# Performance work log

Measured on AMD Instinct MI355X. Metric: run time of the kernel, lower is better.

The kernel has to match this reference:

```python
import jax, jax.numpy as jnp
import numpy as np

MEM_LEN = 1024
EPS = 1e-5


def _layer_norm(x, g, b):
    mu = jnp.mean(x, axis=-1, keepdims=True)
    var = jnp.mean((x - mu) ** 2, axis=-1, keepdims=True)
    return (x - mu) * jax.lax.rsqrt(var + EPS) * g + b


def _rel_shift(t):
    # t: [B, H, T, L] -> TXL pad->view->slice->view shift
    B, H, T, L = t.shape
    padded = jnp.concatenate([jnp.zeros((B, H, T, 1), t.dtype), t], axis=-1)
    padded = padded.reshape(B, H, L + 1, T)
    return padded[:, :, 1:, :].reshape(B, H, T, L)


def _pos_emb(length, d_model, dtype):
    inv_freq = 1.0 / (10000.0 ** (np.arange(0, d_model, 2, dtype=np.float32) / d_model))
    pos_seq = np.arange(length - 1, -1, -1, dtype=np.float32)
    sin_inp = np.outer(pos_seq, inv_freq)
    pe = np.concatenate([np.sin(sin_inp), np.cos(sin_inp)], axis=-1)
    return jnp.asarray(pe, dtype=dtype)


def setup_inputs() -> dict:
    key = jax.random.key(0)
    ks = jax.random.split(key, 12)
    B, T, M, D, H, Dff = 4, 1024, 1024, 1024, 16, 4096
    dh = D // H
    s = 1.0 / np.sqrt(D)
    return {
        "x": jax.random.normal(ks[0], (B, T, D), jnp.float32),
        "mem": jax.random.normal(ks[1], (B, M, D), jnp.float32),
        "Wq": jax.random.normal(ks[2], (D, D), jnp.float32) * s,
        "Wk": jax.random.normal(ks[3], (D, D), jnp.float32) * s,
        "Wv": jax.random.normal(ks[4], (D, D), jnp.float32) * s,
        "Wr": jax.random.normal(ks[5], (D, D), jnp.float32) * s,
        "Wo": jax.random.normal(ks[6], (D, D), jnp.float32) * s,
        "bias_u": jax.random.normal(ks[7], (H, dh), jnp.float32) * 0.02,
        "bias_v": jax.random.normal(ks[8], (H, dh), jnp.float32) * 0.02,
        "ln1_g": jnp.ones((D,), jnp.float32),
        "ln1_b": jnp.zeros((D,), jnp.float32),
        "ln2_g": jnp.ones((D,), jnp.float32),
        "ln2_b": jnp.zeros((D,), jnp.float32),
        "W1": jax.random.normal(ks[9], (D, Dff), jnp.float32) * s,
        "b1": jnp.zeros((Dff,), jnp.float32),
        "W2": jax.random.normal(ks[10], (Dff, D), jnp.float32) * (1.0 / np.sqrt(Dff)),
        "b2": jnp.zeros((D,), jnp.float32),
    }


def reference(x, mem, Wq, Wk, Wv, Wr, Wo, bias_u, bias_v,
              ln1_g, ln1_b, ln2_g, ln2_b, W1, b1, W2, b2):
    B, T, D = x.shape
    M = mem.shape[1]
    H, dh = bias_u.shape
    L = T + M
    scale = 1.0 / np.sqrt(dh)

    residual = x
    xn = _layer_norm(x, ln1_g, ln1_b)

    cat = jnp.concatenate([mem_n := mem, xn], axis=1) if False else jnp.concatenate([mem, xn], axis=1)
    # NOTE: torch concatenates raw memory states (not re-normalized) with norm_x.
    k = (cat @ Wk).reshape(B, L, H, dh).transpose(0, 2, 1, 3)      # [B,H,L,dh]
    v = (cat @ Wv).reshape(B, L, H, dh).transpose(0, 2, 1, 3)      # [B,H,L,dh]
    q = (xn @ Wq).reshape(B, T, H, dh).transpose(0, 2, 1, 3)       # [B,H,T,dh]

    pe = _pos_emb(L, D, x.dtype)                                   # [L,D]
    r = (pe @ Wr).reshape(L, H, dh).transpose(1, 0, 2)             # [H,L,dh]

    content = jnp.einsum("bhid,bhjd->bhij", q + bias_u[None, :, None, :], k)
    rel = jnp.einsum("bhid,hjd->bhij", q + bias_v[None, :, None, :], r)
    rel = _rel_shift(rel)

    attn = jax.nn.softmax((content + rel) * scale, axis=-1)        # [B,H,T,L]
    out = jnp.einsum("bhij,bhjd->bhid", attn, v)                   # [B,H,T,dh]
    out = out.transpose(0, 2, 1, 3).reshape(B, T, D) @ Wo

    x2 = residual + out
    xf = _layer_norm(x2, ln2_g, ln2_b)
    ff = jax.nn.gelu(xf @ W1 + b1, approximate=False) @ W2 + b2
    y = x2 + ff

    new_mem = jax.lax.stop_gradient(
        jnp.concatenate([mem, residual], axis=1)[:, -MEM_LEN:])
    return y, new_mem
```

## Files before the change

kernel.cpp:

```cpp
#include <hip/hip_runtime.h>
#include <hip/hip_bf16.h>

typedef short bf16x8 __attribute__((ext_vector_type(8)));
typedef float f32x4 __attribute__((ext_vector_type(4)));
typedef unsigned short u16;

__device__ __forceinline__ float bf2f(u16 u) {
    union { unsigned int i; float f; } x; x.i = ((unsigned int)u) << 16; return x.f;
}
__device__ __forceinline__ u16 f2bf(float f) {
    union { float f; unsigned int i; } x; x.f = f;
    unsigned int r = x.i + 0x7fff + ((x.i >> 16) & 1);
    return (u16)(r >> 16);
}
__device__ __forceinline__ f32x4 mfma16(bf16x8 a, bf16x8 b, f32x4 c) {
    return __builtin_amdgcn_mfma_f32_16x16x32_bf16(a, b, c, 0, 0, 0);
}
#define GLL16(lds_base, gsrc) \
    __builtin_amdgcn_global_load_lds((const __attribute__((address_space(1))) void*)(gsrc), \
                                     (__attribute__((address_space(3))) void*)(lds_base), 16, 0, 0)

__global__ __launch_bounds__(256)
void transpose_kernel(const float* __restrict__ in, u16* __restrict__ out, int R, int C) {
    __shared__ float t[32][33];
    const int c0 = blockIdx.x * 32, r0 = blockIdx.y * 32;
    const int tx = threadIdx.x & 31, ty = threadIdx.x >> 5;
#pragma unroll
    for (int i = 0; i < 32; i += 8) t[ty + i][tx] = in[(size_t)(r0 + ty + i) * C + c0 + tx];
    __syncthreads();
#pragma unroll
    for (int i = 0; i < 32; i += 8) out[(size_t)(c0 + ty + i) * R + r0 + tx] = f2bf(t[tx][ty + i]);
}

__global__ __launch_bounds__(256)
void convert_kernel(const float* __restrict__ in, u16* __restrict__ out) {
    const size_t i = ((size_t)blockIdx.x * 256 + threadIdx.x) * 8;
    const float4 a = *(const float4*)(in + i);
    const float4 b = *(const float4*)(in + i + 4);
    bf16x8 o;
    o[0] = (short)f2bf(a.x); o[1] = (short)f2bf(a.y);
    o[2] = (short)f2bf(a.z); o[3] = (short)f2bf(a.w);
    o[4] = (short)f2bf(b.x); o[5] = (short)f2bf(b.y);
    o[6] = (short)f2bf(b.z); o[7] = (short)f2bf(b.w);
    *(bf16x8*)(out + i) = o;
}

__global__ __launch_bounds__(256)
void pe_kernel(u16* __restrict__ pe) {
    const int idx = blockIdx.x * 256 + threadIdx.x;
    const int p = idx >> 10, d = idx & 1023;
    const float pos = (float)(2047 - p);
    const int k = d & 511;
    const float invf = powf(10000.f, ((float)(2 * k)) * (-1.f / 1024.f));
    const float a = pos * invf;
    pe[idx] = f2bf((d < 512) ? sinf(a) : cosf(a));
}

__global__ __launch_bounds__(256)
void ln_kernel(const float* __restrict__ inp, const float* __restrict__ gg,
               const float* __restrict__ bb, u16* __restrict__ outp) {
    const int row = blockIdx.x * 4 + (threadIdx.x >> 6);
    const int l = threadIdx.x & 63;
    const size_t base = (size_t)row * 1024 + l * 16;
    float v[16];
    const float4* p4 = (const float4*)(inp + base);
#pragma unroll
    for (int j = 0; j < 4; ++j) {
        float4 f = p4[j];
        v[j*4+0] = f.x; v[j*4+1] = f.y; v[j*4+2] = f.z; v[j*4+3] = f.w;
    }
    float s = 0.f, s2 = 0.f;
#pragma unroll
    for (int j = 0; j < 16; ++j) { s += v[j]; s2 += v[j] * v[j]; }
#pragma unroll
    for (int off = 1; off < 64; off <<= 1) {
        s += __shfl_xor(s, off, 64);
        s2 += __shfl_xor(s2, off, 64);
    }
    const float mu = s * 0.0009765625f;
    const float var = s2 * 0.0009765625f - mu * mu;
    const float rs = rsqrtf(var + 1e-5f);
#pragma unroll
    for (int j = 0; j < 16; ++j)
        outp[base + j] = f2bf((v[j] - mu) * rs * gg[l * 16 + j] + bb[l * 16 + j]);
}

template<int EPI, bool CATA>
__global__ __launch_bounds__(256)
void gemm_kernel(const u16* __restrict__ A, const u16* __restrict__ A2,
                 const u16* __restrict__ Wt, void* __restrict__ outp,
                 u16* __restrict__ out2, const float* __restrict__ cb1,
                 const float* __restrict__ cb2, const float* __restrict__ residp,
                 int Mdim, int Ndim, int Kdim) {
    __shared__ __attribute__((aligned(16))) u16 As[128 * 32];
    __shared__ __attribute__((aligned(16))) u16 Bs[128 * 32];
    const int tid = threadIdx.x;
    const int w = tid >> 6, l = tid & 63;
    const int wr = w >> 1, wc = w & 1;
    const int m0 = blockIdx.x * 128, n0 = blockIdx.y * 128;
    f32x4 acc[4][4] = {};

    for (int k0 = 0; k0 < Kdim; k0 += 32) {
        __syncthreads();
#pragma unroll
        for (int p = 0; p < 2; ++p) {
            const int ebase = (p * 4 + w) * 512;
            const int e = ebase + l * 8;
            const int row = e >> 5, colk = e & 31;
            const u16* srcA;
            if (CATA) {
                const int rr = m0 + row;
                const int bb_ = rr >> 11, pos = rr & 2047;
                srcA = (pos < 1024 ? A + ((size_t)(bb_ * 1024 + pos)) * 1024
                                   : A2 + ((size_t)(bb_ * 1024 + pos - 1024)) * 1024)
                       + (k0 + colk);
            } else {
                srcA = A + (size_t)(m0 + row) * Kdim + (k0 + colk);
            }
            const u16* srcB = Wt + (size_t)(n0 + row) * Kdim + (k0 + colk);
            GLL16(&As[ebase], srcA);
            GLL16(&Bs[ebase], srcB);
        }
        __syncthreads();
        bf16x8 af[4], bfr[4];
#pragma unroll
        for (int mi = 0; mi < 4; ++mi)
            af[mi] = *(const bf16x8*)&As[(wr * 64 + mi * 16 + (l & 15)) * 32 + (l >> 4) * 8];
#pragma unroll
        for (int ni = 0; ni < 4; ++ni)
            bfr[ni] = *(const bf16x8*)&Bs[(wc * 64 + ni * 16 + (l & 15)) * 32 + (l >> 4) * 8];
#pragma unroll
        for (int mi = 0; mi < 4; ++mi)
#pragma unroll
            for (int ni = 0; ni < 4; ++ni)
                acc[mi][ni] = mfma16(af[mi], bfr[ni], acc[mi][ni]);
    }

#pragma unroll
    for (int mi = 0; mi < 4; ++mi)
#pragma unroll
        for (int ni = 0; ni < 4; ++ni)
#pragma unroll
            for (int rg = 0; rg < 4; ++rg) {
                const int row = m0 + wr * 64 + mi * 16 + (l >> 4) * 4 + rg;
                const int col = n0 + wc * 64 + ni * 16 + (l & 15);
                const size_t idx = (size_t)row * Ndim + col;
                const float v = acc[mi][ni][rg];
                if (EPI == 0) {
                    ((u16*)outp)[idx] = f2bf(v);
                } else if (EPI == 1) {
                    ((u16*)outp)[idx] = f2bf(v + cb1[col]);
                    out2[idx] = f2bf(v + cb2[col]);
                } else if (EPI == 2) {
                    ((float*)outp)[idx] = v + residp[idx];
                } else if (EPI == 3) {
                    const float t = v + cb1[col];
                    ((u16*)outp)[idx] = f2bf(0.5f * t * (1.f + erff(t * 0.70710678118654752f)));
                } else {
                    ((float*)outp)[idx] = v + cb1[col] + residp[idx];
                }
            }
}

template<int EPI>
__global__ __launch_bounds__(256)
void gemm64_kernel(const u16* __restrict__ A, const u16* __restrict__ Wt,
                   void* __restrict__ outp, u16* __restrict__ out2,
                   const float* __restrict__ cb1, const float* __restrict__ cb2,
                   const float* __restrict__ residp,
                   int Mdim, int Ndim, int Kdim) {
    __shared__ __attribute__((aligned(16))) u16 As[64 * 32];
    __shared__ __attribute__((aligned(16))) u16 Bs[128 * 32];
    const int tid = threadIdx.x;
    const int w = tid >> 6, l = tid & 63;
    const int m0 = blockIdx.x * 64, n0 = blockIdx.y * 128;
    f32x4 acc[4][2] = {};

    for (int k0 = 0; k0 < Kdim; k0 += 32) {
        __syncthreads();
        {
            const int e = (w * 64 + l) * 8;
            const int row = e >> 5, colk = e & 31;
            GLL16(&As[w * 512], A + (size_t)(m0 + row) * Kdim + (k0 + colk));
        }
#pragma unroll
        for (int p = 0; p < 2; ++p) {
            const int ebase = (p * 4 + w) * 512;
            const int e = ebase + l * 8;
            const int row = e >> 5, colk = e & 31;
            GLL16(&Bs[ebase], Wt + (size_t)(n0 + row) * Kdim + (k0 + colk));
        }
        __syncthreads();
        bf16x8 af[4], bfr[2];
#pragma unroll
        for (int mi = 0; mi < 4; ++mi)
            af[mi] = *(const bf16x8*)&As[(mi * 16 + (l & 15)) * 32 + (l >> 4) * 8];
#pragma unroll
        for (int ni = 0; ni < 2; ++ni)
            bfr[ni] = *(const bf16x8*)&Bs[(w * 32 + ni * 16 + (l & 15)) * 32 + (l >> 4) * 8];
#pragma unroll
        for (int mi = 0; mi < 4; ++mi)
#pragma unroll
            for (int ni = 0; ni < 2; ++ni)
                acc[mi][ni] = mfma16(af[mi], bfr[ni], acc[mi][ni]);
    }

#pragma unroll
    for (int mi = 0; mi < 4; ++mi)
#pragma unroll
        for (int ni = 0; ni < 2; ++ni)
#pragma unroll
            for (int rg = 0; rg < 4; ++rg) {
                const int row = m0 + mi * 16 + (l >> 4) * 4 + rg;
                const int col = n0 + w * 32 + ni * 16 + (l & 15);
                const size_t idx = (size_t)row * Ndim + col;
                const float v = acc[mi][ni][rg];
                if (EPI == 0) {
                    ((u16*)outp)[idx] = f2bf(v);
                } else if (EPI == 1) {
                    ((u16*)outp)[idx] = f2bf(v + cb1[col]);
                    out2[idx] = f2bf(v + cb2[col]);
                } else if (EPI == 2) {
                    ((float*)outp)[idx] = v + residp[idx];
                } else {
                    ((float*)outp)[idx] = v + cb1[col] + residp[idx];
                }
            }
}

__global__ __launch_bounds__(256)
void gemm_kv_kernel(const u16* __restrict__ A, const u16* __restrict__ A2,
                    const u16* __restrict__ WtK, const u16* __restrict__ WtV,
                    u16* __restrict__ outK, u16* __restrict__ outV) {
    __shared__ __attribute__((aligned(16))) u16 As[128 * 32];
    __shared__ __attribute__((aligned(16))) u16 Bk[128 * 32];
    __shared__ __attribute__((aligned(16))) u16 Bv[128 * 32];
    const int tid = threadIdx.x;
    const int w = tid >> 6, l = tid & 63;
    const int wr = w >> 1, wc = w & 1;
    const int m0 = blockIdx.x * 128, n0 = blockIdx.y * 128;
    f32x4 acck[4][4] = {};
    f32x4 accv[4][4] = {};

    for (int k0 = 0; k0 < 1024; k0 += 32) {
        __syncthreads();
#pragma unroll
        for (int p = 0; p < 2; ++p) {
            const int ebase = (p * 4 + w) * 512;
            const int e = ebase + l * 8;
            const int row = e >> 5, colk = e & 31;
            const int rr = m0 + row;
            const int bb_ = rr >> 11, pos = rr & 2047;
            const u16* srcA = (pos < 1024 ? A + ((size_t)(bb_ * 1024 + pos)) * 1024
                                          : A2 + ((size_t)(bb_ * 1024 + pos - 1024)) * 1024)
                              + (k0 + colk);
            GLL16(&As[ebase], srcA);
            GLL16(&Bk[ebase], WtK + (size_t)(n0 + row) * 1024 + (k0 + colk));
            GLL16(&Bv[ebase], WtV + (size_t)(n0 + row) * 1024 + (k0 + colk));
        }
        __syncthreads();
        bf16x8 af[4], bkf[4], bvf[4];
#pragma unroll
        for (int mi = 0; mi < 4; ++mi)
            af[mi] = *(const bf16x8*)&As[(wr * 64 + mi * 16 + (l & 15)) * 32 + (l >> 4) * 8];
#pragma unroll
        for (int ni = 0; ni < 4; ++ni) {
            const int off = (wc * 64 + ni * 16 + (l & 15)) * 32 + (l >> 4) * 8;
            bkf[ni] = *(const bf16x8*)&Bk[off];
            bvf[ni] = *(const bf16x8*)&Bv[off];
        }
#pragma unroll
        for (int mi = 0; mi < 4; ++mi)
#pragma unroll
            for (int ni = 0; ni < 4; ++ni) {
                acck[mi][ni] = mfma16(af[mi], bkf[ni], acck[mi][ni]);
                accv[mi][ni] = mfma16(af[mi], bvf[ni], accv[mi][ni]);
            }
    }

#pragma unroll
    for (int mi = 0; mi < 4; ++mi)
#pragma unroll
        for (int ni = 0; ni < 4; ++ni)
#pragma unroll
            for (int rg = 0; rg < 4; ++rg) {
                const int row = m0 + wr * 64 + mi * 16 + (l >> 4) * 4 + rg;
                const int col = n0 + wc * 64 + ni * 16 + (l & 15);
                const size_t idx = (size_t)row * 1024 + col;
                outK[idx] = f2bf(acck[mi][ni][rg]);
                outV[idx] = f2bf(accv[mi][ni][rg]);
            }
}

__global__ __launch_bounds__(256, 2)
void attn_kernel(const u16* __restrict__ qu, const u16* __restrict__ qv,
                 const u16* __restrict__ kcat, const u16* __restrict__ vcat,
                 const u16* __restrict__ rbuf, u16* __restrict__ outp) {
    constexpr int T = 1024, L = 2048, MM = 1024;
    __shared__ __attribute__((aligned(16))) u16 KtL[64 * 64];
    __shared__ __attribute__((aligned(16))) u16 RmL[128 * 64];
    __shared__ __attribute__((aligned(16))) u16 RwL[128 * 64];
    __shared__ __attribute__((aligned(16))) u16 Vt[64][72];
    __shared__ __attribute__((aligned(16))) u16 Pl[4][16][72];
    const int bid = blockIdx.x;
    const int g = (bid & 7) + 8 * (bid >> 7);
    const int it = (bid >> 3) & 15;
    const int h = g & 15, b = g >> 4;
    const int i0 = it * 64;
    const int tid = threadIdx.x;
    const int w = tid >> 6, l = tid & 63;
    const int lg = l >> 4, ll = l & 15;
    const int iw0 = i0 + w * 16;
    const int l8 = l >> 3;
    const int ssrc = ((l & 7) * 8) ^ (l8 << 3);
    const int sA = (lg * 8) ^ ((ll & 7) << 3);
    const int sB = (lg * 8 + 32) ^ ((ll & 7) << 3);

    bf16x8 quf[2], qvf[2];
    const int qc = h * 64 + lg * 8;
    {
        const size_t qrow = (size_t)(b * T + iw0 + ll);
        quf[0] = *(const bf16x8*)&qu[qrow * 1024 + qc];
        quf[1] = *(const bf16x8*)&qu[qrow * 1024 + qc + 32];
        qvf[0] = *(const bf16x8*)&qv[qrow * 1024 + qc];
        qvf[1] = *(const bf16x8*)&qv[qrow * 1024 + qc + 32];
    }
    const int r2 = iw0 + ll + 1;
    const size_t qrow2 = (size_t)(b * T + (r2 < T ? r2 : T - 1));
    const u16* kb = kcat + (size_t)b * L * 1024 + h * 64;
    const u16* vb = vcat + (size_t)b * L * 1024 + h * 64;
    const u16* rb = rbuf + h * 64;

    f32x4 o_acc[4] = {};
    float m_run[4] = {-1e30f, -1e30f, -1e30f, -1e30f};
    float l_run[4] = {0.f, 0.f, 0.f, 0.f};
    const int vjq = tid & 15, vdg = tid >> 4;

    for (int jt = 0; jt < 32; ++jt) {
        const int j0 = jt * 64;
        const bool main_blk = (j0 <= MM + i0 + 63);
        const bool wrap_blk = (j0 + 63 >= MM + i0 + 2);
        __syncthreads();
#pragma unroll
        for (int p = 0; p < 2; ++p) {
            const int k8 = w * 2 + p;
            GLL16(&KtL[k8 * 512], kb + (size_t)(j0 + k8 * 8 + l8) * 1024 + ssrc);
        }
        if (main_blk) {
            const long bm = (long)j0 + T - i0 - 64;
#pragma unroll
            for (int p = 0; p < 4; ++p) {
                const int k8 = w * 4 + p;
                GLL16(&RmL[k8 * 512], rb + (long)(bm + k8 * 8 + l8) * 1024 + ssrc);
            }
        }
        if (wrap_blk) {
            const long bw_ = (long)j0 - MM - i0 - 65;
#pragma unroll
            for (int p = 0; p < 4; ++p) {
                const int k8 = w * 4 + p;
                GLL16(&RwL[k8 * 512], rb + (long)(bw_ + k8 * 8 + l8) * 1024 + ssrc);
            }
        }
        {
            const u16* srcv = vb + (size_t)(j0 + vjq * 4) * 1024 + vdg * 4;
            const ushort4 r0 = *(const ushort4*)(srcv);
            const ushort4 r1 = *(const ushort4*)(srcv + 1024);
            const ushort4 r2w = *(const ushort4*)(srcv + 2048);
            const ushort4 r3 = *(const ushort4*)(srcv + 3072);
            const ushort4 c0 = {r0.x, r1.x, r2w.x, r3.x};
            const ushort4 c1 = {r0.y, r1.y, r2w.y, r3.y};
            const ushort4 c2 = {r0.z, r1.z, r2w.z, r3.z};
            const ushort4 c3 = {r0.w, r1.w, r2w.w, r3.w};
            *(ushort4*)&Vt[vdg * 4 + 0][vjq * 4] = c0;
            *(ushort4*)&Vt[vdg * 4 + 1][vjq * 4] = c1;
            *(ushort4*)&Vt[vdg * 4 + 2][vjq * 4] = c2;
            *(ushort4*)&Vt[vdg * 4 + 3][vjq * 4] = c3;
        }
        __syncthreads();

        f32x4 sv[4];
        __builtin_amdgcn_s_setprio(1);
#pragma unroll
        for (int ns = 0; ns < 4; ++ns) {
            const int rowb = (ns * 16 + ll) * 64;
            f32x4 a = {0.f, 0.f, 0.f, 0.f};
            a = mfma16(quf[0], *(const bf16x8*)&KtL[rowb + sA], a);
            a = mfma16(quf[1], *(const bf16x8*)&KtL[rowb + sB], a);
            sv[ns] = a;
        }
        __builtin_amdgcn_s_setprio(0);

        if (j0 <= MM + iw0 + 15) {
            const int trb = 48 - 16 * w;
            f32x4 gb[5];
#pragma unroll
            for (int cs = 0; cs < 5; ++cs) {
                const int rowb = (trb + cs * 16 + ll) * 64;
                f32x4 a = {0.f, 0.f, 0.f, 0.f};
                a = mfma16(qvf[0], *(const bf16x8*)&RmL[rowb + sA], a);
                a = mfma16(qvf[1], *(const bf16x8*)&RmL[rowb + sB], a);
                gb[cs] = a;
            }
#pragma unroll
            for (int r = 0; r < 4; ++r) {
                const int i_loc = lg * 4 + r;
                const int srcl = (l & 48) | ((ll + 15 - i_loc) & 15);
                const float sh0 = __shfl(gb[0][r], srcl, 64);
                const float sh1 = __shfl(gb[1][r], srcl, 64);
                const float sh2 = __shfl(gb[2][r], srcl, 64);
                const float sh3 = __shfl(gb[3][r], srcl, 64);
                const float sh4 = __shfl(gb[4][r], srcl, 64);
                const bool hi = (ll > i_loc);
                const int thr = MM + iw0 + i_loc - j0;
                const float e0 = hi ? sh1 : sh0;
                const float e1 = hi ? sh2 : sh1;
                const float e2 = hi ? sh3 : sh2;
                const float e3 = hi ? sh4 : sh3;
                if (ll <= thr)      sv[0][r] += e0;
                if (16 + ll <= thr) sv[1][r] += e1;
                if (32 + ll <= thr) sv[2][r] += e2;
                if (48 + ll <= thr) sv[3][r] += e3;
            }
        }
        if (j0 + 63 >= MM + iw0 + 2) {
            const bf16x8 qv2f0 = *(const bf16x8*)&qv[qrow2 * 1024 + qc];
            const bf16x8 qv2f1 = *(const bf16x8*)&qv[qrow2 * 1024 + qc + 32];
            const int trb = 48 - 16 * w;
            f32x4 gb[5];
#pragma unroll
            for (int cs = 0; cs < 5; ++cs) {
                const int rowb = (trb + cs * 16 + ll) * 64;
                f32x4 a = {0.f, 0.f, 0.f, 0.f};
                a = mfma16(qv2f0, *(const bf16x8*)&RwL[rowb + sA], a);
                a = mfma16(qv2f1, *(const bf16x8*)&RwL[rowb + sB], a);
                gb[cs] = a;
            }
#pragma unroll
            for (int r = 0; r < 4; ++r) {
                const int i_loc = lg * 4 + r;
                const int srcl = (l & 48) | ((ll + 15 - i_loc) & 15);
                const float sh0 = __shfl(gb[0][r], srcl, 64);
                const float sh1 = __shfl(gb[1][r], srcl, 64);
                const float sh2 = __shfl(gb[2][r], srcl, 64);
                const float sh3 = __shfl(gb[3][r], srcl, 64);
                const float sh4 = __shfl(gb[4][r], srcl, 64);
                const bool hi = (ll > i_loc);
                const int thr2 = MM + iw0 + i_loc - j0 + 2;
                const float e0 = hi ? sh1 : sh0;
                const float e1 = hi ? sh2 : sh1;
                const float e2 = hi ? sh3 : sh2;
                const float e3 = hi ? sh4 : sh3;
                if (ll >= thr2)      sv[0][r] += e0;
                if (16 + ll >= thr2) sv[1][r] += e1;
                if (32 + ll >= thr2) sv[2][r] += e2;
                if (48 + ll >= thr2) sv[3][r] += e3;
            }
        }

#pragma unroll
        for (int r = 0; r < 4; ++r) {
            const int i_loc = lg * 4 + r;
            const float s0 = sv[0][r] * 0.125f, s1 = sv[1][r] * 0.125f;
            const float s2 = sv[2][r] * 0.125f, s3 = sv[3][r] * 0.125f;
            float pm = fmaxf(fmaxf(s0, s1), fmaxf(s2, s3));
            pm = fmaxf(pm, __shfl_xor(pm, 1, 64));
            pm = fmaxf(pm, __shfl_xor(pm, 2, 64));
            pm = fmaxf(pm, __shfl_xor(pm, 4, 64));
            pm = fmaxf(pm, __shfl_xor(pm, 8, 64));
            const float mnew = fmaxf(m_run[r], pm);
            const float alpha = __expf(m_run[r] - mnew);
            const float p0 = __expf(s0 - mnew), p1 = __expf(s1 - mnew);
            const float p2 = __expf(s2 - mnew), p3 = __expf(s3 - mnew);
            Pl[w][i_loc][0 * 16 + ll] = f2bf(p0);
            Pl[w][i_loc][1 * 16 + ll] = f2bf(p1);
            Pl[w][i_loc][2 * 16 + ll] = f2bf(p2);
            Pl[w][i_loc][3 * 16 + ll] = f2bf(p3);
            float ps = p0 + p1 + p2 + p3;
            ps += __shfl_xor(ps, 1, 64);
            ps += __shfl_xor(ps, 2, 64);
            ps += __shfl_xor(ps, 4, 64);
            ps += __shfl_xor(ps, 8, 64);
            l_run[r] = l_run[r] * alpha + ps;
            m_run[r] = mnew;
#pragma unroll
            for (int ns = 0; ns < 4; ++ns) o_acc[ns][r] *= alpha;
        }

        __builtin_amdgcn_s_setprio(1);
        const bf16x8 ap0 = *(const bf16x8*)&Pl[w][ll][lg * 8];
        const bf16x8 ap1 = *(const bf16x8*)&Pl[w][ll][32 + lg * 8];
#pragma unroll
        for (int ns = 0; ns < 4; ++ns) {
            const bf16x8 bv0 = *(const bf16x8*)&Vt[ns * 16 + ll][lg * 8];
            const bf16x8 bv1 = *(const bf16x8*)&Vt[ns * 16 + ll][32 + lg * 8];
            o_acc[ns] = mfma16(ap0, bv0, o_acc[ns]);
            o_acc[ns] = mfma16(ap1, bv1, o_acc[ns]);
        }
        __builtin_amdgcn_s_setprio(0);
    }

#pragma unroll
    for (int ns = 0; ns < 4; ++ns)
#pragma unroll
        for (int r = 0; r < 4; ++r) {
            const int row = iw0 + lg * 4 + r;
            outp[(size_t)(b * T + row) * 1024 + h * 64 + ns * 16 + ll] =
                f2bf(o_acc[ns][r] / l_run[r]);
        }
}

extern "C" void kernel_launch(void* const* d_in, const int* in_sizes, int n_in,
                              void* d_out, int out_size, void* d_ws, size_t ws_size,
                              hipStream_t stream) {
    const float* x    = (const float*)d_in[0];
    const float* mem  = (const float*)d_in[1];
    const float* Wq   = (const float*)d_in[2];
    const float* Wk   = (const float*)d_in[3];
    const float* Wv   = (const float*)d_in[4];
    const float* Wr   = (const float*)d_in[5];
    const float* Wo   = (const float*)d_in[6];
    const float* bu   = (const float*)d_in[7];
    const float* bv   = (const float*)d_in[8];
    const float* ln1g = (const float*)d_in[9];
    const float* ln1b = (const float*)d_in[10];
    const float* ln2g = (const float*)d_in[11];
    const float* ln2b = (const float*)d_in[12];
    const float* W1   = (const float*)d_in[13];
    const float* b1   = (const float*)d_in[14];
    const float* W2   = (const float*)d_in[15];
    const float* b2   = (const float*)d_in[16];

    float* y_out   = (float*)d_out;
    float* mem_out = (float*)d_out + 4194304;

    char* dob = (char*)d_out;
    u16* attno     = (u16*)(dob + 0);
    u16* pe        = (u16*)(dob + (size_t)8  * 1048576);
    u16* rbuf_base = (u16*)(dob + (size_t)12 * 1048576);
    u16* rbuf      = rbuf_base + 80 * 1024;
    char* dw = dob + (size_t)16 * 1048576 + 524288;
    u16* WqT = (u16*)(dw);
    u16* WkT = (u16*)(dw + (size_t)2 * 1048576);
    u16* WvT = (u16*)(dw + (size_t)4 * 1048576);
    u16* WrT = (u16*)(dw + (size_t)6 * 1048576);
    u16* WoT = (u16*)(dw + (size_t)8 * 1048576);

    char* ws = (char*)d_ws;
    const size_t MB = 1u << 20;
    u16*  xn    = (u16*)(ws + 0 * MB);
    u16*  x2n   = (u16*)(ws + 0 * MB);
    u16*  W2T   = (u16*)(ws + 0 * MB);
    u16*  qu    = (u16*)(ws + 8 * MB);
    float* x2f  = (float*)(ws + 8 * MB);
    u16*  qv    = (u16*)(ws + 16 * MB);
    u16*  kcat  = (u16*)(ws + 24 * MB);
    u16*  ffh   = (u16*)(ws + 24 * MB);
    u16*  vcat  = (u16*)(ws + 40 * MB);
    u16*  memb  = (u16*)(ws + 56 * MB);
    u16*  W1T   = (u16*)(ws + 56 * MB);

    transpose_kernel<<<dim3(32, 32), 256, 0, stream>>>(Wq, WqT, 1024, 1024);
    transpose_kernel<<<dim3(32, 32), 256, 0, stream>>>(Wk, WkT, 1024, 1024);
    transpose_kernel<<<dim3(32, 32), 256, 0, stream>>>(Wv, WvT, 1024, 1024);
    transpose_kernel<<<dim3(32, 32), 256, 0, stream>>>(Wr, WrT, 1024, 1024);
    transpose_kernel<<<dim3(32, 32), 256, 0, stream>>>(Wo, WoT, 1024, 1024);
    pe_kernel<<<8192, 256, 0, stream>>>(pe);
    convert_kernel<<<2048, 256, 0, stream>>>(mem, memb);
    ln_kernel<<<1024, 256, 0, stream>>>(x, ln1g, ln1b, xn);
    gemm64_kernel<0><<<dim3(32, 8), 256, 0, stream>>>(pe, WrT, rbuf, nullptr, nullptr, nullptr, nullptr, 2048, 1024, 1024);
    gemm64_kernel<1><<<dim3(64, 8), 256, 0, stream>>>(xn, WqT, qu, qv, bu, bv, nullptr, 4096, 1024, 1024);
    gemm_kv_kernel<<<dim3(64, 8), 256, 0, stream>>>(memb, xn, WkT, WvT, kcat, vcat);
    attn_kernel<<<1024, 256, 0, stream>>>(qu, qv, kcat, vcat, rbuf, attno);
    gemm64_kernel<2><<<dim3(64, 8), 256, 0, stream>>>(attno, WoT, x2f, nullptr, nullptr, nullptr, x, 4096, 1024, 1024);
    transpose_kernel<<<dim3(128, 32), 256, 0, stream>>>(W1, W1T, 1024, 4096);
    hipMemcpyAsync(mem_out, x, (size_t)4194304 * 4, hipMemcpyDeviceToDevice, stream);
    ln_kernel<<<1024, 256, 0, stream>>>(x2f, ln2g, ln2b, x2n);
    gemm_kernel<3, false><<<dim3(32, 32), 256, 0, stream>>>(x2n, nullptr, W1T, ffh, nullptr, b1, nullptr, nullptr, 4096, 4096, 1024);
    transpose_kernel<<<dim3(32, 128), 256, 0, stream>>>(W2, W2T, 4096, 1024);
    gemm64_kernel<4><<<dim3(64, 8), 256, 0, stream>>>(ffh, W2T, y_out, nullptr, b2, nullptr, x2f, 4096, 1024, 4096);
    (void)in_sizes; (void)n_in; (void)out_size; (void)ws_size;
}
```

Measured before the change: 564.9 us.

## Batch weight transposes, compute softmax row-sum via MFMA, permute P/V layout

Merges five separate weight-transpose launches into one 3D-grid launch to cut launch overhead. In attention, the per-row softmax denominator is now accumulated by an extra MFMA against a ones vector instead of shuffle reductions, removing four cross-lane shuffles per row per tile. P is written as packed 4-wide stores with a permuted column order, and the V transpose load is permuted to match so the PV product stays consistent. This relies on the matching permutation of P and V columns and adds two MFMAs per tile.

```diff
diff --git a/kernel.cpp b/kernel.cpp
--- a/kernel.cpp
+++ b/kernel.cpp
@@ -19,6 +19,31 @@
 #define GLL16(lds_base, gsrc) \
     __builtin_amdgcn_global_load_lds((const __attribute__((address_space(1))) void*)(gsrc), \
                                      (__attribute__((address_space(3))) void*)(lds_base), 16, 0, 0)
+
+__global__ __launch_bounds__(256)
+void transpose5_kernel(const float* __restrict__ s0, const float* __restrict__ s1,
+                       const float* __restrict__ s2, const float* __restrict__ s3,
+                       const float* __restrict__ s4,
+                       u16* __restrict__ d0, u16* __restrict__ d1,
+                       u16* __restrict__ d2, u16* __restrict__ d3,
+                       u16* __restrict__ d4) {
+    const float* in; u16* out;
+    switch (blockIdx.z) {
+        case 0: in = s0; out = d0; break;
+        case 1: in = s1; out = d1; break;
+        case 2: in = s2; out = d2; break;
+        case 3: in = s3; out = d3; break;
+        default: in = s4; out = d4; break;
+    }
+    __shared__ float t[32][33];
+    const int c0 = blockIdx.x * 32, r0 = blockIdx.y * 32;
+    const int tx = threadIdx.x & 31, ty = threadIdx.x >> 5;
+#pragma unroll
+    for (int i = 0; i < 32; i += 8) t[ty + i][tx] = in[(size_t)(r0 + ty + i) * 1024 + c0 + tx];
+    __syncthreads();
+#pragma unroll
+    for (int i = 0; i < 32; i += 8) out[(size_t)(c0 + ty + i) * 1024 + r0 + tx] = f2bf(t[tx][ty + i]);
+}
 
 __global__ __launch_bounds__(256)
 void transpose_kernel(const float* __restrict__ in, u16* __restrict__ out, int R, int C) {
@@ -332,8 +357,10 @@
     const u16* rb = rbuf + h * 64;
 
     f32x4 o_acc[4] = {};
+    f32x4 o_sum = {0.f, 0.f, 0.f, 0.f};
     float m_run[4] = {-1e30f, -1e30f, -1e30f, -1e30f};
-    float l_run[4] = {0.f, 0.f, 0.f, 0.f};
+    const bf16x8 onesb = {(short)0x3F80, (short)0x3F80, (short)0x3F80, (short)0x3F80,
+                          (short)0x3F80, (short)0x3F80, (short)0x3F80, (short)0x3F80};
     const int vjq = tid & 15, vdg = tid >> 4;
 
     for (int jt = 0; jt < 32; ++jt) {
@@ -363,11 +390,11 @@
             }
         }
         {
-            const u16* srcv = vb + (size_t)(j0 + vjq * 4) * 1024 + vdg * 4;
+            const u16* srcv = vb + (size_t)(j0 + vjq) * 1024 + vdg * 4;
             const ushort4 r0 = *(const ushort4*)(srcv);
-            const ushort4 r1 = *(const ushort4*)(srcv + 1024);
-            const ushort4 r2w = *(const ushort4*)(srcv + 2048);
-            const ushort4 r3 = *(const ushort4*)(srcv + 3072);
+            const ushort4 r1 = *(const ushort4*)(srcv + 16 * 1024);
+            const ushort4 r2w = *(const ushort4*)(srcv + 32 * 1024);
+            const ushort4 r3 = *(const ushort4*)(srcv + 48 * 1024);
             const ushort4 c0 = {r0.x, r1.x, r2w.x, r3.x};
             const ushort4 c1 = {r0.y, r1.y, r2w.y, r3.y};
             const ushort4 c2 = {r0.z, r1.z, r2w.z, r3.z};
@@ -472,17 +499,10 @@
             const float alpha = __expf(m_run[r] - mnew);
             const float p0 = __expf(s0 - mnew), p1 = __expf(s1 - mnew);
             const float p2 = __expf(s2 - mnew), p3 = __expf(s3 - mnew);
-            Pl[w][i_loc][0 * 16 + ll] = f2bf(p0);
-            Pl[w][i_loc][1 * 16 + ll] = f2bf(p1);
-            Pl[w][i_loc][2 * 16 + ll] = f2bf(p2);
-            Pl[w][i_loc][3 * 16 + ll] = f2bf(p3);
-            float ps = p0 + p1 + p2 + p3;
-            ps += __shfl_xor(ps, 1, 64);
-            ps += __shfl_xor(ps, 2, 64);
-            ps += __shfl_xor(ps, 4, 64);
-            ps += __shfl_xor(ps, 8, 64);
-            l_run[r] = l_run[r] * alpha + ps;
+            const ushort4 pw = {f2bf(p0), f2bf(p1), f2bf(p2), f2bf(p3)};
+            *(ushort4*)&Pl[w][i_loc][ll * 4] = pw;
             m_run[r] = mnew;
+            o_sum[r] *= alpha;
 #pragma unroll
             for (int ns = 0; ns < 4; ++ns) o_acc[ns][r] *= alpha;
         }
@@ -497,6 +517,8 @@
             o_acc[ns] = mfma16(ap0, bv0, o_acc[ns]);
             o_acc[ns] = mfma16(ap1, bv1, o_acc[ns]);
         }
+        o_sum = mfma16(ap0, onesb, o_sum);
+        o_sum = mfma16(ap1, onesb, o_sum);
         __builtin_amdgcn_s_setprio(0);
     }
 
@@ -506,7 +528,7 @@
         for (int r = 0; r < 4; ++r) {
             const int row = iw0 + lg * 4 + r;
             outp[(size_t)(b * T + row) * 1024 + h * 64 + ns * 16 + ll] =
-                f2bf(o_acc[ns][r] / l_run[r]);
+                f2bf(o_acc[ns][r] / o_sum[r]);
         }
 }
 
@@ -560,11 +582,8 @@
     u16*  memb  = (u16*)(ws + 56 * MB);
     u16*  W1T   = (u16*)(ws + 56 * MB);
 
-    transpose_kernel<<<dim3(32, 32), 256, 0, stream>>>(Wq, WqT, 1024, 1024);
-    transpose_kernel<<<dim3(32, 32), 256, 0, stream>>>(Wk, WkT, 1024, 1024);
-    transpose_kernel<<<dim3(32, 32), 256, 0, stream>>>(Wv, WvT, 1024, 1024);
-    transpose_kernel<<<dim3(32, 32), 256, 0, stream>>>(Wr, WrT, 1024, 1024);
-    transpose_kernel<<<dim3(32, 32), 256, 0, stream>>>(Wo, WoT, 1024, 1024);
+    transpose5_kernel<<<dim3(32, 32, 5), 256, 0, stream>>>(Wq, Wk, Wv, Wr, Wo,
+                                                           WqT, WkT, WvT, WrT, WoT);
     pe_kernel<<<8192, 256, 0, stream>>>(pe);
     convert_kernel<<<2048, 256, 0, stream>>>(mem, memb);
     ln_kernel<<<1024, 256, 0, stream>>>(x, ln1g, ln1b, xn);
```

Result: faster. 538.8 us (-4.6%).
